# Kernel tuning notes

Measured on AMD Instinct MI355X. Metric: run time of the kernel, lower is better.

Reference implementation:

```python
import jax, jax.numpy as jnp
import numpy as np
import math

NUM_HEADS = 16
EPS = 1e-5

# Single-step spikingjelly LIFNode(tau=2.0, v_threshold=1.0, v_reset=0.0):
#   v = (x - 0)/tau = x/2 ; spike = heaviside(v - 1) = (x >= 2)
@jax.custom_vjp
def lif(x):
    return (x >= 2.0).astype(x.dtype)

def _lif_fwd(x):
    return (x >= 2.0).astype(x.dtype), x

def _lif_bwd(x, g):
    # sigmoid surrogate (alpha=4) on v - v_th, chained through dv/dx = 1/tau = 0.5
    s = jax.nn.sigmoid(4.0 * (0.5 * x - 1.0))
    return (g * (4.0 * s * (1.0 - s)) * 0.5,)

lif.defvjp(_lif_fwd, _lif_bwd)

def layernorm(x, gamma, beta):
    mu = jnp.mean(x, axis=-1, keepdims=True)
    var = jnp.var(x, axis=-1, keepdims=True)
    return (x - mu) * jax.lax.rsqrt(var + EPS) * gamma + beta

def mish(x):
    return x * jnp.tanh(jax.nn.softplus(x))

def setup_inputs() -> dict:
    key = jax.random.key(0)
    ks = jax.random.split(key, 8)
    B, Sq, Skv, dQ, dK, dV = 8, 1024, 1024, 1024, 1024, 1024
    def xavier_normal(k, shape):
        std = math.sqrt(2.0 / (shape[0] + shape[1]))
        return jax.random.normal(k, shape, jnp.float32) * std
    return {
        "Q": jax.random.normal(ks[0], (B, Sq, dQ), jnp.float32) * 2.0,
        "K": jax.random.normal(ks[1], (B, Skv, dK), jnp.float32) * 2.0,
        "adj_mask": (jax.random.uniform(ks[2], (B, 1, Sq, Skv)) < 0.7).astype(jnp.float32),
        "Wq": xavier_normal(ks[3], (dV, dQ)), "bq": jnp.zeros((dV,), jnp.float32),
        "Wk": xavier_normal(ks[4], (dV, dK)), "bk": jnp.zeros((dV,), jnp.float32),
        "Wv": xavier_normal(ks[5], (dV, dK)), "bv": jnp.zeros((dV,), jnp.float32),
        "Wo": xavier_normal(ks[6], (dV, dV)), "bo": jnp.zeros((dV,), jnp.float32),
        "g_q": jnp.ones((dV,), jnp.float32), "be_q": jnp.zeros((dV,), jnp.float32),
        "g_k": jnp.ones((dV,), jnp.float32), "be_k": jnp.zeros((dV,), jnp.float32),
    }

def reference(Q, K, adj_mask, Wq, bq, Wk, bk, Wv, bv, Wo, bo, g_q, be_q, g_k, be_k):
    B, Sq, _ = Q.shape
    Skv = K.shape[1]
    dV = Wq.shape[0]
    hd = dV // NUM_HEADS
    # LIF-gated projections (eval mode: dropout off)
    q = lif(layernorm(lif(Q) @ Wq.T + bq, g_q, be_q))          # [B,Sq,dV] binary
    v = lif(K) @ Wv.T + bv                                      # fc_v(k_lif(K))
    k = lif(layernorm(lif(K) @ Wk.T + bk, g_k, be_k))          # K(k_norm(fc_k(v_lif(K))))
    q = q.reshape(B, Sq, NUM_HEADS, hd).transpose(0, 2, 1, 3)  # [B,H,Sq,hd]
    k = k.reshape(B, Skv, NUM_HEADS, hd).transpose(0, 2, 1, 3)
    v = v.reshape(B, Skv, NUM_HEADS, hd).transpose(0, 2, 1, 3)
    scores = jnp.einsum('bhqd,bhkd->bhqk', q, k) / math.sqrt(hd)
    scores = scores * adj_mask                                  # multiplicative mask
    w = jax.nn.softmax(scores, axis=-1)
    out = jnp.einsum('bhqk,bhkd->bhqd', w, v)
    out = out.transpose(0, 2, 1, 3).reshape(B, Sq, dV)
    o = out @ Wo.T + bo
    return out + mish(o)
```

## Files before the change

kernel.cpp:

```cpp
#include <hip/hip_runtime.h>
#include <hip/hip_bf16.h>

typedef __attribute__((ext_vector_type(4))) float fx4;
typedef __attribute__((ext_vector_type(8))) short bv8;
typedef unsigned int u32;
typedef unsigned short u16;
typedef __hip_bfloat16 bf16;

#define DEVI static __device__ __forceinline__

static constexpr int NBATCH = 8;
static constexpr int SEQ = 1024;
static constexpr int DM  = 1024;
static constexpr int NH  = 16;
static constexpr int MROWS = NBATCH * SEQ;
static constexpr size_t SZ = (size_t)MROWS * DM;

DEVI void gl16(const void* g, void* l) {
  __builtin_amdgcn_global_load_lds((const __attribute__((address_space(1))) void*)g,
                                   (__attribute__((address_space(3))) void*)l, 16, 0, 0);
}
DEVI fx4 mfma_bf16(bv8 a, bv8 b, fx4 c) {
  return __builtin_amdgcn_mfma_f32_16x16x32_bf16(a, b, c, 0, 0, 0);
}

__global__ __launch_bounds__(256) void prep_weights(
    const float* __restrict__ wq, const float* __restrict__ wk,
    const float* __restrict__ wv, const float* __restrict__ wo,
    bf16* __restrict__ qh, bf16* __restrict__ qm, bf16* __restrict__ ql,
    bf16* __restrict__ kh, bf16* __restrict__ km, bf16* __restrict__ kl,
    bf16* __restrict__ vb, bf16* __restrict__ ob)
{
  int i = (blockIdx.x * 256 + threadIdx.x) * 4;
  int w = blockIdx.y;
  const float* src = (w == 0) ? wq : (w == 1) ? wk : (w == 2) ? wv : wo;
  fx4 v = *(const fx4*)&src[i];
  if (w < 2) {
    bf16* hi = (w == 0) ? qh : kh;
    bf16* mi = (w == 0) ? qm : km;
    bf16* lo = (w == 0) ? ql : kl;
#pragma unroll
    for (int j = 0; j < 4; j++) {
      float x = v[j];
      bf16 h = __float2bfloat16(x);
      float r1 = x - __bfloat162float(h);
      bf16 m = __float2bfloat16(r1);
      float r2 = r1 - __bfloat162float(m);
      hi[i + j] = h;
      mi[i + j] = m;
      lo[i + j] = __float2bfloat16(r2);
    }
  } else {
    bf16* dst = (w == 2) ? vb : ob;
#pragma unroll
    for (int j = 0; j < 4; j++) dst[i + j] = __float2bfloat16(v[j]);
  }
}

__global__ __launch_bounds__(256) void spike_kernel(const float* __restrict__ x, u16* __restrict__ o)
{
  size_t i = ((size_t)blockIdx.x * 256 + threadIdx.x) * 4;
  fx4 v = *(const fx4*)&x[i];
  u32 a = (v[0] >= 2.f ? 0x3F80u : 0u) | ((v[1] >= 2.f ? 0x3F80u : 0u) << 16);
  u32 b = (v[2] >= 2.f ? 0x3F80u : 0u) | ((v[3] >= 2.f ? 0x3F80u : 0u) << 16);
  u32* p = (u32*)(o + i);
  p[0] = a; p[1] = b;
}

__global__ __launch_bounds__(256) void maskpack_kernel(const float* __restrict__ m, u32* __restrict__ w)
{
  size_t gid = (size_t)blockIdx.x * 256 + threadIdx.x;
  unsigned long long bal = __ballot(m[gid] != 0.0f);
  int lane = threadIdx.x & 63;
  u32 skv = (u32)(gid & 1023);
  u32 sq  = (u32)((gid >> 10) & 1023);
  u32 b   = (u32)(gid >> 20);
  size_t oidx = (size_t)b * 32768 + (skv >> 5) * 1024 + sq;
  if (lane == 0) w[oidx] = (u32)bal;
  else if (lane == 32) w[oidx] = (u32)(bal >> 32);
}

template<int NB, int EPI>
__global__ __launch_bounds__(256) void gemm_bt(
    const bf16* __restrict__ A, const bf16* __restrict__ B0, const bf16* __restrict__ B1,
    const bf16* __restrict__ B2,
    const float* __restrict__ bias, const float* __restrict__ addsrc,
    float* __restrict__ Cf, bf16* __restrict__ Cb, int K, int N)
{
  __shared__ __attribute__((aligned(16))) bf16 sA[128 * 64];
  __shared__ __attribute__((aligned(16))) bf16 sB[NB * 128 * 64];
  const bf16* Bp[3] = {B0, B1, B2};
  const int tid = threadIdx.x;
  const int lane = tid & 63, wave = tid >> 6;
  const int wr = wave >> 1, wc = wave & 1;
  const int l15 = lane & 15, l4 = lane >> 4;
  const int rowBase = blockIdx.x * 128;
  const int colBase = blockIdx.y * 128;

  fx4 acc[4][4];
#pragma unroll
  for (int m = 0; m < 4; m++) {
#pragma unroll
    for (int n = 0; n < 4; n++) acc[m][n] = fx4{0.f, 0.f, 0.f, 0.f};
  }

  for (int kt = 0; kt < K; kt += 64) {
#pragma unroll
    for (int i = 0; i < 4; i++) {
      int c = i * 256 + tid;
      int r = c >> 3, cb = (c & 7) * 8;
      gl16(A + (size_t)(rowBase + r) * K + kt + cb, &sA[c * 8]);
    }
#pragma unroll
    for (int b = 0; b < NB; b++) {
#pragma unroll
      for (int i = 0; i < 4; i++) {
        int c = i * 256 + tid;
        int r = c >> 3, cb = (c & 7) * 8;
        gl16(Bp[b] + (size_t)(colBase + r) * K + kt + cb, &sB[b * 128 * 64 + c * 8]);
      }
    }
    __syncthreads();
#pragma unroll
    for (int kk = 0; kk < 2; kk++) {
      bv8 af[4];
#pragma unroll
      for (int m = 0; m < 4; m++)
        af[m] = *(const bv8*)&sA[(wr * 64 + m * 16 + l15) * 64 + kk * 32 + l4 * 8];
#pragma unroll
      for (int b = 0; b < NB; b++) {
#pragma unroll
        for (int n = 0; n < 4; n++) {
          bv8 bfr = *(const bv8*)&sB[b * 128 * 64 + (wc * 64 + n * 16 + l15) * 64 + kk * 32 + l4 * 8];
#pragma unroll
          for (int m = 0; m < 4; m++) acc[m][n] = mfma_bf16(af[m], bfr, acc[m][n]);
        }
      }
    }
    __syncthreads();
  }
#pragma unroll
  for (int n = 0; n < 4; n++) {
    int col = colBase + wc * 64 + n * 16 + l15;
    float bvv = bias[col];
#pragma unroll
    for (int m = 0; m < 4; m++) {
      int row0 = rowBase + wr * 64 + m * 16 + l4 * 4;
#pragma unroll
      for (int r = 0; r < 4; r++) {
        size_t idx = (size_t)(row0 + r) * N + col;
        float val = acc[m][n][r] + bvv;
        if (EPI == 0) {
          Cf[idx] = val;
        } else if (EPI == 1) {
          Cb[idx] = __float2bfloat16(val);
        } else {
          float sp = log1pf(__expf(val));
          Cf[idx] = addsrc[idx] + val * tanhf(sp);
        }
      }
    }
  }
}

__global__ __launch_bounds__(256) void lnlif_kernel(
    const float* __restrict__ x, const float* __restrict__ g, const float* __restrict__ be,
    u16* __restrict__ out)
{
  __shared__ float red[4];
  const int row = blockIdx.x;
  const int tid = threadIdx.x;
  fx4 v = *(const fx4*)&x[(size_t)row * DM + tid * 4];
  float s = v[0] + v[1] + v[2] + v[3];
#pragma unroll
  for (int off = 1; off < 64; off <<= 1) s += __shfl_xor(s, off, 64);
  if ((tid & 63) == 0) red[tid >> 6] = s;
  __syncthreads();
  float mean = (red[0] + red[1] + red[2] + red[3]) * (1.0f / 1024.0f);
  __syncthreads();
  float d0 = v[0] - mean, d1 = v[1] - mean, d2 = v[2] - mean, d3 = v[3] - mean;
  float ss = d0 * d0 + d1 * d1 + d2 * d2 + d3 * d3;
#pragma unroll
  for (int off = 1; off < 64; off <<= 1) ss += __shfl_xor(ss, off, 64);
  if ((tid & 63) == 0) red[tid >> 6] = ss;
  __syncthreads();
  float var = (red[0] + red[1] + red[2] + red[3]) * (1.0f / 1024.0f);
  float rstd = rsqrtf(var + 1e-5f);
  const int c = tid * 4;
  fx4 gg = *(const fx4*)&g[c];
  fx4 bb = *(const fx4*)&be[c];
  float y0 = d0 * rstd * gg[0] + bb[0];
  float y1 = d1 * rstd * gg[1] + bb[1];
  float y2 = d2 * rstd * gg[2] + bb[2];
  float y3 = d3 * rstd * gg[3] + bb[3];
  u32 a = (y0 >= 2.f ? 0x3F80u : 0u) | ((y1 >= 2.f ? 0x3F80u : 0u) << 16);
  u32 b = (y2 >= 2.f ? 0x3F80u : 0u) | ((y3 >= 2.f ? 0x3F80u : 0u) << 16);
  u32* p = (u32*)(out + (size_t)row * DM + c);
  p[0] = a; p[1] = b;
}

__global__ __launch_bounds__(256) void transpose_v(const bf16* __restrict__ v, bf16* __restrict__ vt)
{
  __shared__ bf16 t[64][72];
  const int tc = blockIdx.x, tr = blockIdx.y, b = blockIdx.z;
  const int tid = threadIdx.x;
  const size_t base = (size_t)b * SEQ * DM;
#pragma unroll
  for (int i = 0; i < 2; i++) {
    int c = i * 256 + tid;
    int r = c >> 3, cg = (c & 7) * 8;
    bv8 val = *(const bv8*)&v[base + (size_t)(tr * 64 + r) * DM + tc * 64 + cg];
#pragma unroll
    for (int j = 0; j < 8; j++) t[r][cg + j] = ((const bf16*)&val)[j];
  }
  __syncthreads();
#pragma unroll
  for (int i = 0; i < 2; i++) {
    int c = i * 256 + tid;
    int r = c >> 3, cg = (c & 7) * 8;
    bf16 tmp[8];
#pragma unroll
    for (int j = 0; j < 8; j++) tmp[j] = t[cg + j][r];
    *(bv8*)&vt[base + (size_t)(tc * 64 + r) * SEQ + tr * 64 + cg] = *(const bv8*)tmp;
  }
}

__global__ __launch_bounds__(256) void attn_kernel(
    const bf16* __restrict__ qb, const bf16* __restrict__ kb, const bf16* __restrict__ vt,
    const u32* __restrict__ mwT, float* __restrict__ of, bf16* __restrict__ ob)
{
  __shared__ __attribute__((aligned(16))) bf16 sK[2][64 * 64];
  __shared__ __attribute__((aligned(16))) bf16 sV[2][64 * 64];
  __shared__ __attribute__((aligned(16))) bf16 sP[4][16 * 64];
  __shared__ __attribute__((aligned(16))) u32 sM[2][128];
  const int qt = blockIdx.x, h = blockIdx.y, b = blockIdx.z;
  const int tid = threadIdx.x, lane = tid & 63, wave = tid >> 6;
  const int l15 = lane & 15, l4 = lane >> 4;
  const size_t qrow0 = (size_t)b * SEQ + qt * 64;
  const bf16* kB = kb + (size_t)b * SEQ * DM + h * 64;
  const bf16* vB = vt + (size_t)b * SEQ * DM + (size_t)(h * 64) * SEQ;
  const u32*  mB = mwT + (size_t)b * 32768 + qt * 64;

  auto STAGE = [&](int t, int buf) {
    const int kvb = t * 64;
#pragma unroll
    for (int i = 0; i < 2; i++) {
      int c = i * 256 + tid;
      int row = c >> 3;
      int sb = ((c & 7) * 16) ^ ((row & 7) << 4);
      gl16(kB + (size_t)(kvb + row) * DM + (sb >> 1), &sK[buf][c * 8]);
      gl16(vB + (size_t)row * SEQ + kvb + (sb >> 1), &sV[buf][c * 8]);
    }
    if (tid < 32) {
      int w = tid >> 4, rg = (tid & 15) * 4;
      uint4 mv = *(const uint4*)&mB[(size_t)(t * 2 + w) * 1024 + rg];
      *(uint4*)&sM[buf][w * 64 + rg] = mv;
    }
  };

  bv8 af[2];
#pragma unroll
  for (int kk = 0; kk < 2; kk++)
    af[kk] = *(const bv8*)&qb[(qrow0 + wave * 16 + l15) * DM + h * 64 + kk * 32 + l4 * 8];

  fx4 acc_o[4];
#pragma unroll
  for (int n = 0; n < 4; n++) acc_o[n] = fx4{0.f, 0.f, 0.f, 0.f};
  float psum[4] = {0.f, 0.f, 0.f, 0.f};

  char* sPw = (char*)sP[wave];
  STAGE(0, 0);

  for (int t = 0; t < 16; t++) {
    const int cur = t & 1;
    asm volatile("s_waitcnt vmcnt(0) lgkmcnt(0)" ::: "memory");
    __builtin_amdgcn_s_barrier();
    if (t < 15) STAGE(t + 1, cur ^ 1);

    const char* sKc = (const char*)sK[cur];
    const char* sVc = (const char*)sV[cur];

    fx4 accs[4];
#pragma unroll
    for (int n = 0; n < 4; n++) accs[n] = fx4{0.f, 0.f, 0.f, 0.f};
    __builtin_amdgcn_s_setprio(1);
#pragma unroll
    for (int kk = 0; kk < 2; kk++) {
#pragma unroll
      for (int n = 0; n < 4; n++) {
        int row = n * 16 + l15;
        bv8 bk8 = *(const bv8*)(sKc + row * 128 + ((kk * 64 + l4 * 16) ^ ((row & 7) << 4)));
        accs[n] = mfma_bf16(af[kk], bk8, accs[n]);
      }
    }
    __builtin_amdgcn_s_setprio(0);

    uint4 m0 = *(const uint4*)&sM[cur][wave * 16 + l4 * 4];
    uint4 m1 = *(const uint4*)&sM[cur][64 + wave * 16 + l4 * 4];
    u32 sh0[4] = {m0.x >> l15, m0.y >> l15, m0.z >> l15, m0.w >> l15};
    u32 sh1[4] = {m1.x >> l15, m1.y >> l15, m1.z >> l15, m1.w >> l15};

#pragma unroll
    for (int n = 0; n < 4; n++) {
#pragma unroll
      for (int r = 0; r < 4; r++) {
        float e = exp2f(accs[n][r] * 0.18033688011112042f);
        u32 s = (n < 2) ? sh0[r] : sh1[r];
        float p = ((s >> ((n & 1) * 16)) & 1u) ? e : 1.0f;
        psum[r] += p;
        int pr = l4 * 4 + r;
        int cb = (n * 16 + l15) * 2;
        *(bf16*)(sPw + pr * 128 + (cb ^ ((pr & 7) << 4))) = __float2bfloat16(p);
      }
    }

    __builtin_amdgcn_s_setprio(1);
#pragma unroll
    for (int kk = 0; kk < 2; kk++) {
      bv8 pa = *(const bv8*)(sPw + l15 * 128 + ((kk * 64 + l4 * 16) ^ ((l15 & 7) << 4)));
#pragma unroll
      for (int n = 0; n < 4; n++) {
        int row = n * 16 + l15;
        bv8 bv8v = *(const bv8*)(sVc + row * 128 + ((kk * 64 + l4 * 16) ^ ((row & 7) << 4)));
        acc_o[n] = mfma_bf16(pa, bv8v, acc_o[n]);
      }
    }
    __builtin_amdgcn_s_setprio(0);
  }

#pragma unroll
  for (int r = 0; r < 4; r++) {
    float t2 = psum[r];
    t2 += __shfl_xor(t2, 1, 64);
    t2 += __shfl_xor(t2, 2, 64);
    t2 += __shfl_xor(t2, 4, 64);
    t2 += __shfl_xor(t2, 8, 64);
    float inv = 1.0f / t2;
    size_t row = qrow0 + wave * 16 + (l4 << 2) + r;
#pragma unroll
    for (int n = 0; n < 4; n++) {
      size_t idx = row * DM + h * 64 + n * 16 + l15;
      float val = acc_o[n][r] * inv;
      of[idx] = val;
      ob[idx] = __float2bfloat16(val);
    }
  }
}

extern "C" void kernel_launch(void* const* d_in, const int* in_sizes, int n_in,
                              void* d_out, int out_size, void* d_ws, size_t ws_size,
                              hipStream_t stream) {
  (void)in_sizes; (void)n_in; (void)out_size; (void)ws_size;
  const float* Q    = (const float*)d_in[0];
  const float* Kin  = (const float*)d_in[1];
  const float* mask = (const float*)d_in[2];
  const float* Wq   = (const float*)d_in[3];
  const float* bq   = (const float*)d_in[4];
  const float* Wk   = (const float*)d_in[5];
  const float* bk   = (const float*)d_in[6];
  const float* Wv   = (const float*)d_in[7];
  const float* bv   = (const float*)d_in[8];
  const float* Wo   = (const float*)d_in[9];
  const float* bo   = (const float*)d_in[10];
  const float* g_q  = (const float*)d_in[11];
  const float* be_q = (const float*)d_in[12];
  const float* g_k  = (const float*)d_in[13];
  const float* be_k = (const float*)d_in[14];
  float* out = (float*)d_out;

  char* w = (char*)d_ws;
  size_t off = 0;
  auto alloc = [&](size_t bytes) -> char* {
    char* p = w + off;
    off += (bytes + 255) & ~(size_t)255;
    return p;
  };
  bf16* q_spike = (bf16*)alloc(SZ * 2);
  bf16* k_spike = (bf16*)alloc(SZ * 2);
  float* xq     = (float*)alloc(SZ * 4);
  float* xk     = (float*)alloc(SZ * 4);
  bf16* vb_     = (bf16*)alloc(SZ * 2);
  bf16* vtb     = (bf16*)alloc(SZ * 2);
  u32* mwords   = (u32*)alloc(SZ / 32 * 4);
  bf16* whq = (bf16*)alloc((size_t)DM * DM * 2);
  bf16* wmq = (bf16*)alloc((size_t)DM * DM * 2);
  bf16* wlq = (bf16*)alloc((size_t)DM * DM * 2);
  bf16* whk = (bf16*)alloc((size_t)DM * DM * 2);
  bf16* wmk = (bf16*)alloc((size_t)DM * DM * 2);
  bf16* wlk = (bf16*)alloc((size_t)DM * DM * 2);
  bf16* wvb = (bf16*)alloc((size_t)DM * DM * 2);
  bf16* wob = (bf16*)alloc((size_t)DM * DM * 2);
  bf16* qbn = q_spike;
  bf16* kbn = k_spike;
  float* attn_out = xq;
  bf16* attn_outb = (bf16*)xk;

  prep_weights<<<dim3(DM * DM / 1024, 4), 256, 0, stream>>>(Wq, Wk, Wv, Wo,
                                                            whq, wmq, wlq, whk, wmk, wlk, wvb, wob);
  spike_kernel<<<SZ / 1024, 256, 0, stream>>>(Q, (u16*)q_spike);
  spike_kernel<<<SZ / 1024, 256, 0, stream>>>(Kin, (u16*)k_spike);
  maskpack_kernel<<<SZ / 256, 256, 0, stream>>>(mask, mwords);

  gemm_bt<3, 0><<<dim3(64, 8), 256, 0, stream>>>(q_spike, whq, wmq, wlq, bq, nullptr, xq, nullptr, DM, DM);
  gemm_bt<3, 0><<<dim3(64, 8), 256, 0, stream>>>(k_spike, whk, wmk, wlk, bk, nullptr, xk, nullptr, DM, DM);
  gemm_bt<1, 1><<<dim3(64, 8), 256, 0, stream>>>(k_spike, wvb, nullptr, nullptr, bv, nullptr, nullptr, vb_, DM, DM);

  lnlif_kernel<<<MROWS, 256, 0, stream>>>(xq, g_q, be_q, (u16*)qbn);
  lnlif_kernel<<<MROWS, 256, 0, stream>>>(xk, g_k, be_k, (u16*)kbn);
  transpose_v<<<dim3(16, 16, NBATCH), 256, 0, stream>>>(vb_, vtb);

  attn_kernel<<<dim3(16, NH, NBATCH), 256, 0, stream>>>(qbn, kbn, vtb, mwords, attn_out, attn_outb);

  gemm_bt<1, 2><<<dim3(64, 8), 256, 0, stream>>>(attn_outb, wob, nullptr, nullptr, bo, attn_out, out, nullptr, DM, DM);
}
```

Baseline: 495.1 us.

## Concatenate split weights along K, fuse V transpose into GEMM epilogue

The hi/mid/lo bf16 split weights are stored contiguously along K (3072 wide), so the projection GEMM runs one B tile per K-step over three times as many steps instead of loading three B tiles per step. The A tile is re-read with the K index wrapped modulo 1024. The V projection epilogue now writes transposed bf16 output directly, which removes the separate transpose kernel and its buffer. The mish epilogue is rewritten algebraically with a single exp instead of log1p and tanh. Side effects are smaller shared memory per block, more loop iterations with more barriers, strided 8-byte stores in the V epilogue, and possible overflow in the new mish form for large inputs.

```diff
diff --git a/kernel.cpp b/kernel.cpp
--- a/kernel.cpp
+++ b/kernel.cpp
@@ -27,8 +27,7 @@
 __global__ __launch_bounds__(256) void prep_weights(
     const float* __restrict__ wq, const float* __restrict__ wk,
     const float* __restrict__ wv, const float* __restrict__ wo,
-    bf16* __restrict__ qh, bf16* __restrict__ qm, bf16* __restrict__ ql,
-    bf16* __restrict__ kh, bf16* __restrict__ km, bf16* __restrict__ kl,
+    bf16* __restrict__ qe, bf16* __restrict__ ke,
     bf16* __restrict__ vb, bf16* __restrict__ ob)
 {
   int i = (blockIdx.x * 256 + threadIdx.x) * 4;
@@ -36,9 +35,10 @@
   const float* src = (w == 0) ? wq : (w == 1) ? wk : (w == 2) ? wv : wo;
   fx4 v = *(const fx4*)&src[i];
   if (w < 2) {
-    bf16* hi = (w == 0) ? qh : kh;
-    bf16* mi = (w == 0) ? qm : km;
-    bf16* lo = (w == 0) ? ql : kl;
+    bf16* dst = (w == 0) ? qe : ke;
+    int col = i >> 10, k = i & 1023;
+    size_t base = (size_t)col * 3072 + k;
+    bf16 hi[4], mi[4], lo[4];
 #pragma unroll
     for (int j = 0; j < 4; j++) {
       float x = v[j];
@@ -46,14 +46,17 @@
       float r1 = x - __bfloat162float(h);
       bf16 m = __float2bfloat16(r1);
       float r2 = r1 - __bfloat162float(m);
-      hi[i + j] = h;
-      mi[i + j] = m;
-      lo[i + j] = __float2bfloat16(r2);
-    }
+      hi[j] = h; mi[j] = m; lo[j] = __float2bfloat16(r2);
+    }
+    *(uint2*)&dst[base]        = *(const uint2*)hi;
+    *(uint2*)&dst[base + 1024] = *(const uint2*)mi;
+    *(uint2*)&dst[base + 2048] = *(const uint2*)lo;
   } else {
     bf16* dst = (w == 2) ? vb : ob;
-#pragma unroll
-    for (int j = 0; j < 4; j++) dst[i + j] = __float2bfloat16(v[j]);
+    bf16 t[4];
+#pragma unroll
+    for (int j = 0; j < 4; j++) t[j] = __float2bfloat16(v[j]);
+    *(uint2*)&dst[i] = *(const uint2*)t;
   }
 }
 
@@ -80,16 +83,14 @@
   else if (lane == 32) w[oidx] = (u32)(bal >> 32);
 }
 
-template<int NB, int EPI>
+template<int EPI>
 __global__ __launch_bounds__(256) void gemm_bt(
-    const bf16* __restrict__ A, const bf16* __restrict__ B0, const bf16* __restrict__ B1,
-    const bf16* __restrict__ B2,
+    const bf16* __restrict__ A, const bf16* __restrict__ B,
     const float* __restrict__ bias, const float* __restrict__ addsrc,
     float* __restrict__ Cf, bf16* __restrict__ Cb, int K, int N)
 {
   __shared__ __attribute__((aligned(16))) bf16 sA[128 * 64];
-  __shared__ __attribute__((aligned(16))) bf16 sB[NB * 128 * 64];
-  const bf16* Bp[3] = {B0, B1, B2};
+  __shared__ __attribute__((aligned(16))) bf16 sB[128 * 64];
   const int tid = threadIdx.x;
   const int lane = tid & 63, wave = tid >> 6;
   const int wr = wave >> 1, wc = wave & 1;
@@ -105,20 +106,18 @@
   }
 
   for (int kt = 0; kt < K; kt += 64) {
+    const int ka = kt & 1023;
 #pragma unroll
     for (int i = 0; i < 4; i++) {
       int c = i * 256 + tid;
       int r = c >> 3, cb = (c & 7) * 8;
-      gl16(A + (size_t)(rowBase + r) * K + kt + cb, &sA[c * 8]);
-    }
-#pragma unroll
-    for (int b = 0; b < NB; b++) {
-#pragma unroll
-      for (int i = 0; i < 4; i++) {
-        int c = i * 256 + tid;
-        int r = c >> 3, cb = (c & 7) * 8;
-        gl16(Bp[b] + (size_t)(colBase + r) * K + kt + cb, &sB[b * 128 * 64 + c * 8]);
-      }
+      gl16(A + (size_t)(rowBase + r) * 1024 + ka + cb, &sA[c * 8]);
+    }
+#pragma unroll
+    for (int i = 0; i < 4; i++) {
+      int c = i * 256 + tid;
+      int r = c >> 3, cb = (c & 7) * 8;
+      gl16(B + (size_t)(colBase + r) * K + kt + cb, &sB[c * 8]);
     }
     __syncthreads();
 #pragma unroll
@@ -128,13 +127,10 @@
       for (int m = 0; m < 4; m++)
         af[m] = *(const bv8*)&sA[(wr * 64 + m * 16 + l15) * 64 + kk * 32 + l4 * 8];
 #pragma unroll
-      for (int b = 0; b < NB; b++) {
-#pragma unroll
-        for (int n = 0; n < 4; n++) {
-          bv8 bfr = *(const bv8*)&sB[b * 128 * 64 + (wc * 64 + n * 16 + l15) * 64 + kk * 32 + l4 * 8];
-#pragma unroll
-          for (int m = 0; m < 4; m++) acc[m][n] = mfma_bf16(af[m], bfr, acc[m][n]);
-        }
+      for (int n = 0; n < 4; n++) {
+        bv8 bfr = *(const bv8*)&sB[(wc * 64 + n * 16 + l15) * 64 + kk * 32 + l4 * 8];
+#pragma unroll
+        for (int m = 0; m < 4; m++) acc[m][n] = mfma_bf16(af[m], bfr, acc[m][n]);
       }
     }
     __syncthreads();
@@ -146,17 +142,25 @@
 #pragma unroll
     for (int m = 0; m < 4; m++) {
       int row0 = rowBase + wr * 64 + m * 16 + l4 * 4;
-#pragma unroll
-      for (int r = 0; r < 4; r++) {
-        size_t idx = (size_t)(row0 + r) * N + col;
-        float val = acc[m][n][r] + bvv;
-        if (EPI == 0) {
-          Cf[idx] = val;
-        } else if (EPI == 1) {
-          Cb[idx] = __float2bfloat16(val);
-        } else {
-          float sp = log1pf(__expf(val));
-          Cf[idx] = addsrc[idx] + val * tanhf(sp);
+      if (EPI == 3) {
+        bf16 t[4];
+#pragma unroll
+        for (int r = 0; r < 4; r++) t[r] = __float2bfloat16(acc[m][n][r] + bvv);
+        size_t idx = (size_t)(row0 >> 10) * SEQ * DM + (size_t)col * SEQ + (row0 & 1023);
+        *(uint2*)&Cb[idx] = *(const uint2*)t;
+      } else {
+#pragma unroll
+        for (int r = 0; r < 4; r++) {
+          size_t idx = (size_t)(row0 + r) * N + col;
+          float val = acc[m][n][r] + bvv;
+          if (EPI == 0) {
+            Cf[idx] = val;
+          } else {
+            float u = __expf(val);
+            float num = u * (u + 2.0f);
+            float mish = val * num / (num + 2.0f);
+            Cf[idx] = addsrc[idx] + mish;
+          }
         }
       }
     }
@@ -197,32 +201,6 @@
   u32 b = (y2 >= 2.f ? 0x3F80u : 0u) | ((y3 >= 2.f ? 0x3F80u : 0u) << 16);
   u32* p = (u32*)(out + (size_t)row * DM + c);
   p[0] = a; p[1] = b;
-}
-
-__global__ __launch_bounds__(256) void transpose_v(const bf16* __restrict__ v, bf16* __restrict__ vt)
-{
-  __shared__ bf16 t[64][72];
-  const int tc = blockIdx.x, tr = blockIdx.y, b = blockIdx.z;
-  const int tid = threadIdx.x;
-  const size_t base = (size_t)b * SEQ * DM;
-#pragma unroll
-  for (int i = 0; i < 2; i++) {
-    int c = i * 256 + tid;
-    int r = c >> 3, cg = (c & 7) * 8;
-    bv8 val = *(const bv8*)&v[base + (size_t)(tr * 64 + r) * DM + tc * 64 + cg];
-#pragma unroll
-    for (int j = 0; j < 8; j++) t[r][cg + j] = ((const bf16*)&val)[j];
-  }
-  __syncthreads();
-#pragma unroll
-  for (int i = 0; i < 2; i++) {
-    int c = i * 256 + tid;
-    int r = c >> 3, cg = (c & 7) * 8;
-    bf16 tmp[8];
-#pragma unroll
-    for (int j = 0; j < 8; j++) tmp[j] = t[cg + j][r];
-    *(bv8*)&vt[base + (size_t)(tc * 64 + r) * SEQ + tr * 64 + cg] = *(const bv8*)tmp;
-  }
 }
 
 __global__ __launch_bounds__(256) void attn_kernel(
@@ -379,15 +357,10 @@
   bf16* k_spike = (bf16*)alloc(SZ * 2);
   float* xq     = (float*)alloc(SZ * 4);
   float* xk     = (float*)alloc(SZ * 4);
-  bf16* vb_     = (bf16*)alloc(SZ * 2);
   bf16* vtb     = (bf16*)alloc(SZ * 2);
   u32* mwords   = (u32*)alloc(SZ / 32 * 4);
-  bf16* whq = (bf16*)alloc((size_t)DM * DM * 2);
-  bf16* wmq = (bf16*)alloc((size_t)DM * DM * 2);
-  bf16* wlq = (bf16*)alloc((size_t)DM * DM * 2);
-  bf16* whk = (bf16*)alloc((size_t)DM * DM * 2);
-  bf16* wmk = (bf16*)alloc((size_t)DM * DM * 2);
-  bf16* wlk = (bf16*)alloc((size_t)DM * DM * 2);
+  bf16* wqe = (bf16*)alloc((size_t)DM * DM * 3 * 2);
+  bf16* wke = (bf16*)alloc((size_t)DM * DM * 3 * 2);
   bf16* wvb = (bf16*)alloc((size_t)DM * DM * 2);
   bf16* wob = (bf16*)alloc((size_t)DM * DM * 2);
   bf16* qbn = q_spike;
@@ -395,21 +368,19 @@
   float* attn_out = xq;
   bf16* attn_outb = (bf16*)xk;
 
-  prep_weights<<<dim3(DM * DM / 1024, 4), 256, 0, stream>>>(Wq, Wk, Wv, Wo,
-                                                            whq, wmq, wlq, whk, wmk, wlk, wvb, wob);
+  prep_weights<<<dim3(DM * DM / 1024, 4), 256, 0, stream>>>(Wq, Wk, Wv, Wo, wqe, wke, wvb, wob);
   spike_kernel<<<SZ / 1024, 256, 0, stream>>>(Q, (u16*)q_spike);
   spike_kernel<<<SZ / 1024, 256, 0, stream>>>(Kin, (u16*)k_spike);
   maskpack_kernel<<<SZ / 256, 256, 0, stream>>>(mask, mwords);
 
-  gemm_bt<3, 0><<<dim3(64, 8), 256, 0, stream>>>(q_spike, whq, wmq, wlq, bq, nullptr, xq, nullptr, DM, DM);
-  gemm_bt<3, 0><<<dim3(64, 8), 256, 0, stream>>>(k_spike, whk, wmk, wlk, bk, nullptr, xk, nullptr, DM, DM);
-  gemm_bt<1, 1><<<dim3(64, 8), 256, 0, stream>>>(k_spike, wvb, nullptr, nullptr, bv, nullptr, nullptr, vb_, DM, DM);
+  gemm_bt<0><<<dim3(64, 8), 256, 0, stream>>>(q_spike, wqe, bq, nullptr, xq, nullptr, 3072, DM);
+  gemm_bt<0><<<dim3(64, 8), 256, 0, stream>>>(k_spike, wke, bk, nullptr, xk, nullptr, 3072, DM);
+  gemm_bt<3><<<dim3(64, 8), 256, 0, stream>>>(k_spike, wvb, bv, nullptr, nullptr, vtb, 1024, DM);
 
   lnlif_kernel<<<MROWS, 256, 0, stream>>>(xq, g_q, be_q, (u16*)qbn);
   lnlif_kernel<<<MROWS, 256, 0, stream>>>(xk, g_k, be_k, (u16*)kbn);
-  transpose_v<<<dim3(16, 16, NBATCH), 256, 0, stream>>>(vb_, vtb);
 
   attn_kernel<<<dim3(16, NH, NBATCH), 256, 0, stream>>>(qbn, kbn, vtb, mwords, attn_out, attn_outb);
 
-  gemm_bt<1, 2><<<dim3(64, 8), 256, 0, stream>>>(attn_outb, wob, nullptr, nullptr, bo, attn_out, out, nullptr, DM, DM);
-}
+  gemm_bt<2><<<dim3(64, 8), 256, 0, stream>>>(attn_outb, wob, bo, attn_out, out, nullptr, 1024, DM);
+}
```

Result: slower. 505.3 us (+2.1%).
